# Kernel tuning notes

Hardware: AMD Instinct MI355X
Metric: run time of the kernel (lower is better)

Reference implementation:

```python
import jax, jax.numpy as jnp
import numpy as np
from functools import partial

B, N, T = 4, 10000, 128
E = 160000
H, C = 4, 64            # heads, out_channels per head
GAT_DIM = H * C         # 256
NEG_SLOPE = 0.2


def conv1d(x, w, b):
    # x: (M, Cin, L), w: (Cout, Cin, K), 'same' padding (pad=1 for k=3)
    y = jax.lax.conv_general_dilated(x, w, window_strides=(1,), padding=[(1, 1)],
                                     dimension_numbers=('NCH', 'OIH', 'NCH'))
    return y + b[None, :, None]


def maxpool2(x):
    # kernel=2, stride=2 over last axis
    return jax.lax.reduce_window(x, -jnp.inf, jax.lax.max,
                                 (1, 1, 2), (1, 1, 2), 'VALID')


def gat_layer_single(x, src, dst, W, att_s, att_d, bias):
    # x: (N, Fin); PyG GATConv with concat=True, self-loops already appended to src/dst
    n = x.shape[0]
    xl = (x @ W).reshape(n, H, C)                       # (N, H, C)
    a_s = jnp.sum(xl * att_s[None], axis=-1)            # (N, H)
    a_d = jnp.sum(xl * att_d[None], axis=-1)            # (N, H)
    e = jax.nn.leaky_relu(a_s[src] + a_d[dst], NEG_SLOPE)  # (E', H)
    emax = jax.ops.segment_max(e, dst, num_segments=n)     # (N, H)
    ex = jnp.exp(e - emax[dst])
    denom = jax.ops.segment_sum(ex, dst, num_segments=n)   # (N, H)
    alpha = ex / (denom[dst] + 1e-16)                       # (E', H)
    msg = xl[src] * alpha[..., None]                        # (E', H, C)
    out = jax.ops.segment_sum(msg, dst, num_segments=n)     # (N, H, C)
    return out.reshape(n, H * C) + bias


def setup_inputs() -> dict:
    key = jax.random.key(0)
    ks = jax.random.split(key, 24)
    rn = lambda k, sh, fan: jax.random.normal(k, sh, jnp.float32) / np.sqrt(fan)
    inp = {
        'x': jax.random.normal(ks[0], (B, N, T), jnp.float32),
        'edge_index': jax.random.randint(ks[1], (2, E), 0, N, jnp.int64),
        # temporal conv
        'cw1': rn(ks[2], (32, 1, 3), 3), 'cb1': jnp.zeros((32,), jnp.float32),
        'cw2': rn(ks[3], (64, 32, 3), 96), 'cb2': jnp.zeros((64,), jnp.float32),
        # GAT layer 0 (in=64)
        'W0': rn(ks[4], (64, GAT_DIM), 64), 'as0': rn(ks[5], (H, C), C), 'ad0': rn(ks[6], (H, C), C),
        'b0': jnp.zeros((GAT_DIM,), jnp.float32),
        # GAT layer 1 (in=256)
        'W1': rn(ks[7], (GAT_DIM, GAT_DIM), GAT_DIM), 'as1': rn(ks[8], (H, C), C), 'ad1': rn(ks[9], (H, C), C),
        'b1': jnp.zeros((GAT_DIM,), jnp.float32),
        # classification head 256->128->2
        'Wc1': rn(ks[10], (GAT_DIM, 128), GAT_DIM), 'bc1': jnp.zeros((128,), jnp.float32),
        'Wc2': rn(ks[11], (128, 2), 128), 'bc2': jnp.zeros((2,), jnp.float32),
        # attribution head 256->64->1
        'Wa1': rn(ks[12], (GAT_DIM, 64), GAT_DIM), 'ba1': jnp.zeros((64,), jnp.float32),
        'Wa2': rn(ks[13], (64, 1), 64), 'ba2': jnp.zeros((1,), jnp.float32),
    }
    return inp


def reference(x, edge_index, cw1, cb1, cw2, cb2, W0, as0, ad0, b0, W1, as1, ad1, b1,
              Wc1, bc1, Wc2, bc2, Wa1, ba1, Wa2, ba2):
    b, n, t = x.shape
    # ---- temporal conv over all B*N node signals ----
    xf = x.reshape(b * n, 1, t)
    h = jax.nn.relu(conv1d(xf, cw1, cb1))            # (BN, 32, T)
    h = maxpool2(h)                                  # (BN, 32, T//2)
    h = jax.nn.relu(conv1d(h, cw2, cb2))             # (BN, 64, T//2)
    feat = jnp.mean(h, axis=-1).reshape(b, n, 64)    # adaptive_avg_pool1d(1)
    # ---- GAT stack (self-loops appended, PyG default) ----
    src0, dst0 = edge_index[0], edge_index[1]
    loops = jnp.arange(n, dtype=src0.dtype)
    src = jnp.concatenate([src0, loops])
    dst = jnp.concatenate([dst0, loops])
    gat0 = jax.vmap(partial(gat_layer_single, src=src, dst=dst, W=W0, att_s=as0, att_d=ad0, bias=b0))
    gat1 = jax.vmap(partial(gat_layer_single, src=src, dst=dst, W=W1, att_s=as1, att_d=ad1, bias=b1))
    g = jax.nn.relu(gat0(feat))                      # (B, N, 256); dropout = identity (eval)
    g = jax.nn.relu(gat1(g))                         # (B, N, 256)
    # ---- heads ----
    pooled = jnp.mean(g, axis=1)                     # (B, 256)
    logits = jax.nn.relu(pooled @ Wc1 + bc1) @ Wc2 + bc2          # (B, 2)
    attr = jax.nn.sigmoid(jax.nn.relu(g @ Wa1 + ba1) @ Wa2 + ba2)  # (B, N, 1)
    return logits, attr[..., 0]
```

## Files before the change

kernel.cpp:

```cpp
#include <hip/hip_runtime.h>
#include <hip/hip_bf16.h>
#include <math.h>

typedef __hip_bfloat16 bf16;
typedef unsigned short u16;
typedef unsigned int u32;
typedef __attribute__((ext_vector_type(8))) short short8;
typedef __attribute__((ext_vector_type(4))) float f32x4;
typedef __attribute__((ext_vector_type(2))) float f32x2;

#define BATCH 4
#define NNODE 10000
#define TLEN 128
#define NEDGE 160000
#define GDIM 256
#define NHEAD 4

#define S_CW1 0
#define S_CB1 96
#define S_CB2 128
#define S_AS0 192
#define S_AD0 448
#define S_B0  704
#define S_AS1 960
#define S_AD1 1216
#define S_B1  1472
#define S_BC1 1728
#define S_WC2 1856
#define S_BC2 2112
#define S_BA1 2114
#define S_WA2 2178
#define S_BA2 2242
#define S_TOTAL 2243

__device__ __forceinline__ float prelu(float v) { return 0.5f * (v + fabsf(v)); }
__device__ __forceinline__ u16 f2b(float f) {
    union { float f; u32 u; } v; v.f = f;
    u32 r = v.u + 0x7FFF + ((v.u >> 16) & 1);
    return (u16)(r >> 16);
}
__device__ __forceinline__ float u2f(u16 u) {
    union { u32 u; float f; } v; v.u = ((u32)u) << 16;
    return v.f;
}
__device__ __forceinline__ float ldw(const void* p, int off, bool isbf) {
    return isbf ? u2f(((const u16*)p)[off]) : ((const float*)p)[off];
}

__device__ __forceinline__ bool probe_x_bf16(const void* xsrc) {
    int lane = threadIdx.x & 63;
    u16 h = ((const u16*)xsrc)[2 * lane];
    int e = (h >> 7) & 0xFF;
    unsigned long long m = __ballot(e >= 117 && e <= 130);
    return __popcll(m) >= 32;
}
__device__ __forceinline__ bool probe_ei64(const int* ei) {
    int lane = threadIdx.x & 63;
    int v = ei[2 * lane + 1];
    unsigned long long m = __ballot(v == 0);
    return __popcll(m) >= 56;
}

struct WPtrs { const void* p[20]; };

#define PRE_TBLK 665
__global__ __launch_bounds__(256) void k_pre(WPtrs wp, const void* __restrict__ xsrc,
        const int* __restrict__ ei, float* __restrict__ wbuf,
        u16* __restrict__ cw2r, u16* __restrict__ W0t, u16* __restrict__ W1t,
        u16* __restrict__ Wa1t, int* __restrict__ counts) {
    bool isbf = probe_x_bf16(xsrc);
    int b = blockIdx.x;
    if (b >= PRE_TBLK) {
        const int C2[16] = {0,96,128,192,448,704,960,1216,1472,1728,1856,2112,
                            2114,2178,2242,2243};
        const int SRC[15] = {0,1,3,5,6,7,9,10,11,13,14,15,17,18,19};
        int i = (b - PRE_TBLK) * 256 + threadIdx.x;
        if (i >= S_TOTAL) return;
        int j = 14;
        for (int t = 0; t < 15; ++t) { if (i < C2[t + 1]) { j = t; break; } }
        wbuf[i] = ldw(wp.p[SRC[j]], i - C2[j], isbf);
        return;
    }
    int i = b * 256 + threadIdx.x;
    if (i < 6144) {
        int c2 = i / 96, k = i - c2 * 96, s = k >> 5, ci = k & 31;
        cw2r[i] = f2b(ldw(wp.p[2], c2 * 96 + ci * 3 + s, isbf));
    }
    if (i < 16384) {
        int k = i >> 8, c = i & 255;
        W0t[c * 64 + k] = f2b(ldw(wp.p[4], k * 256 + c, isbf));
        int ka = i >> 6, ca = i & 63;
        Wa1t[ca * 256 + ka] = f2b(ldw(wp.p[16], ka * 64 + ca, isbf));
    }
    if (i < 65536) {
        int k = i >> 8, c = i & 255;
        W1t[c * 256 + k] = f2b(ldw(wp.p[8], k * 256 + c, isbf));
    }
    if (i < NEDGE + NNODE) {
        bool ei64 = probe_ei64(ei);
        int dst;
        if (i < NEDGE) dst = ei64 ? ei[2 * (NEDGE + i)] : ei[NEDGE + i];
        else dst = i - NEDGE;
        if (dst >= 0 && dst < NNODE) atomicAdd(&counts[dst], 1);
    }
}

__global__ __launch_bounds__(256) void k_scan1(const int* __restrict__ counts,
        int* __restrict__ cur, int* __restrict__ bsum) {
    __shared__ int buf[256];
    int tid = threadIdx.x;
    int i = blockIdx.x * 256 + tid;
    int v = (i < NNODE) ? counts[i] : 0;
    buf[tid] = v;
    __syncthreads();
    for (int off = 1; off < 256; off <<= 1) {
        int t = (tid >= off) ? buf[tid - off] : 0;
        __syncthreads();
        buf[tid] += t;
        __syncthreads();
    }
    if (i < NNODE) cur[i] = buf[tid];
    if (tid == 255) bsum[blockIdx.x] = buf[255];
}
__global__ __launch_bounds__(256) void k_scan3(const int* __restrict__ counts,
        int* __restrict__ cur, const int* __restrict__ bsum, int* __restrict__ row_ptr) {
    __shared__ int pre_s;
    int tid = threadIdx.x;
    if (tid == 0) {
        int s = 0;
        for (int j = 0; j < blockIdx.x; ++j) s += bsum[j];
        pre_s = s;
    }
    __syncthreads();
    int i = blockIdx.x * 256 + tid;
    if (i >= NNODE) return;
    int incl = cur[i] + pre_s;
    row_ptr[i + 1] = incl;
    cur[i] = incl - counts[i];
    if (i == 0) row_ptr[0] = 0;
}

#define HSTR 40
#define WSTR 96
#define FILL_BLK 665
__global__ __launch_bounds__(256) void k_conv(const void* __restrict__ xsrc,
        const float* __restrict__ wbuf, const u16* __restrict__ cw2r,
        u16* __restrict__ featb, const int* __restrict__ ei,
        int* __restrict__ cur, int* __restrict__ col_src) {
    __shared__ __align__(16) float xs[4][132];
    __shared__ float w1s[96], b1s[32], b2s[64];
    __shared__ __align__(16) u16 w2s[64 * WSTR];
    __shared__ __align__(16) u16 hs[66 * HSTR];
    __shared__ float red2[4][64];

    bool isbf = probe_x_bf16(xsrc);
    int tid = threadIdx.x;
    int wave = tid >> 6, lane = tid & 63;
    int node0 = blockIdx.x * 4;

    {
        int j = tid >> 6, p = (tid & 63) * 2;
        if (isbf) {
            u32 w = ((const u32*)xsrc)[(size_t)node0 * 64 + tid];
            xs[j][1 + p] = u2f((u16)(w & 0xFFFF));
            xs[j][2 + p] = u2f((u16)(w >> 16));
        } else {
            float2 w = ((const float2*)xsrc)[(size_t)node0 * 64 + tid];
            xs[j][1 + p] = w.x;
            xs[j][2 + p] = w.y;
        }
    }
    if (tid < 8) xs[tid >> 1][(tid & 1) ? 129 : 0] = 0.f;
    if (tid < 96) w1s[tid] = wbuf[S_CW1 + tid];
    if (tid < 32) b1s[tid] = wbuf[S_CB1 + tid];
    if (tid < 64) b2s[tid] = wbuf[S_CB2 + tid];
    for (int i = tid; i < 768; i += 256)
        ((short8*)w2s)[i] = ((const short8*)cw2r)[i];
    if (tid < 32) hs[tid] = 0;
    else if (tid < 64) hs[65 * HSTR + (tid - 32)] = 0;
    __syncthreads();

    int d = tid & 15, uu = tid >> 4;
    float wa0 = w1s[6 * d + 0], wa1 = w1s[6 * d + 1], wa2 = w1s[6 * d + 2];
    float wb0 = w1s[6 * d + 3], wb1 = w1s[6 * d + 4], wb2 = w1s[6 * d + 5];
    float ba = b1s[2 * d], bb = b1s[2 * d + 1];
    int m = lane & 15, q = lane >> 4;
    int trow = wave * 16 + m;

    for (int j = 0; j < 4; ++j) {
        const float* xr = &xs[j][0];
        #pragma unroll
        for (int it = 0; it < 4; ++it) {
            int u = uu + 16 * it;
            int t0 = 2 * u;
            float x0 = xr[t0], x1 = xr[t0 + 1], x2 = xr[t0 + 2], x3 = xr[t0 + 3];
            f32x2 A = {x0, x1}, Bv = {x1, x2}, Cv = {x2, x3};
            f32x2 va = {ba, ba}; va += wa0 * A; va += wa1 * Bv; va += wa2 * Cv;
            f32x2 vb = {bb, bb}; vb += wb0 * A; vb += wb1 * Bv; vb += wb2 * Cv;
            float ha = fmaxf(fmaxf(va.x, va.y), 0.f);
            float hb = fmaxf(fmaxf(vb.x, vb.y), 0.f);
            __hip_bfloat162 hp2 = __float22bfloat162_rn(make_float2(ha, hb));
            u32 pack; __builtin_memcpy(&pack, &hp2, 4);
            *(u32*)&hs[(u + 1) * HSTR + 2 * d] = pack;
        }
        __syncthreads();

        short8 afr[3];
        #pragma unroll
        for (int s = 0; s < 3; ++s)
            afr[s] = *(const short8*)&hs[(trow + s) * HSTR + q * 8];
        float psum[4];
        #pragma unroll
        for (int nt = 0; nt < 4; ++nt) {
            int n = nt * 16 + m;
            f32x4 acc = {0.f, 0.f, 0.f, 0.f};
            #pragma unroll
            for (int s = 0; s < 3; ++s) {
                short8 bfr = *(const short8*)&w2s[n * WSTR + s * 32 + q * 8];
                acc = __builtin_amdgcn_mfma_f32_16x16x32_bf16(afr[s], bfr, acc, 0, 0, 0);
            }
            float b2v = b2s[n];
            float scl = prelu(acc[0] + b2v) + prelu(acc[1] + b2v)
                      + prelu(acc[2] + b2v) + prelu(acc[3] + b2v);
            scl += __shfl_xor(scl, 16, 64);
            scl += __shfl_xor(scl, 32, 64);
            psum[nt] = scl;
        }
        if (lane < 16) {
            #pragma unroll
            for (int nt = 0; nt < 4; ++nt)
                red2[wave][nt * 16 + lane] = psum[nt];
        }
        __syncthreads();
        if (tid < 64) {
            float tot = (red2[0][tid] + red2[1][tid] + red2[2][tid] + red2[3][tid]) * (1.f / 64.f);
            int node = node0 + j;
            int bb2 = node / NNODE, nn = node - bb2 * NNODE;
            featb[((size_t)nn * 4 + bb2) * 64 + tid] = f2b(tot);
        }
    }

    if (blockIdx.x < FILL_BLK) {
        bool ei64 = probe_ei64(ei);
        int e = blockIdx.x * 256 + tid;
        if (e < NEDGE + NNODE) {
            int src, dst;
            if (e < NEDGE) {
                if (ei64) { src = ei[2 * e]; dst = ei[2 * (NEDGE + e)]; }
                else      { src = ei[e];     dst = ei[NEDGE + e]; }
            } else {
                src = dst = e - NEDGE;
            }
            if (dst >= 0 && dst < NNODE) {
                int pos = atomicAdd(&cur[dst], 1);
                if (pos >= 0 && pos < NEDGE + NNODE) col_src[pos] = src;
            }
        }
    }
}

template<int K>
__global__ __launch_bounds__(256) void k_gemm(const u16* __restrict__ A,
        const u16* __restrict__ Wt, const float* __restrict__ att_s_w,
        const float* __restrict__ att_d_w, u16* __restrict__ outb,
        float* __restrict__ a_s, float* __restrict__ a_d) {
    int wave = threadIdx.x >> 6, lane = threadIdx.x & 63;
    int row0 = (blockIdx.x * 4 + wave) * 16;
    int m = lane & 15, q = lane >> 4;
    f32x4 acc[16];
    #pragma unroll
    for (int nt = 0; nt < 16; ++nt) acc[nt] = {0.f, 0.f, 0.f, 0.f};
    for (int kc = 0; kc < K; kc += 32) {
        short8 a = *(const short8*)&A[(size_t)(row0 + m) * K + kc + q * 8];
        #pragma unroll
        for (int nt = 0; nt < 16; ++nt) {
            short8 b = *(const short8*)&Wt[(size_t)(nt * 16 + m) * K + kc + q * 8];
            acc[nt] = __builtin_amdgcn_mfma_f32_16x16x32_bf16(a, b, acc[nt], 0, 0, 0);
        }
    }
    #pragma unroll
    for (int nt = 0; nt < 16; ++nt) {
        #pragma unroll
        for (int r = 0; r < 4; ++r)
            outb[(size_t)(row0 + q * 4 + r) * 256 + nt * 16 + m] = f2b(acc[nt][r]);
    }
    float sh_s[4][4] = {{0}}, sh_d[4][4] = {{0}};
    #pragma unroll
    for (int nt = 0; nt < 16; ++nt) {
        int h = nt >> 2;
        int cc = (nt & 3) * 16 + m;
        float asw = att_s_w[h * 64 + cc];
        float adw = att_d_w[h * 64 + cc];
        #pragma unroll
        for (int r = 0; r < 4; ++r) {
            sh_s[h][r] += acc[nt][r] * asw;
            sh_d[h][r] += acc[nt][r] * adw;
        }
    }
    #pragma unroll
    for (int off = 1; off < 16; off <<= 1) {
        #pragma unroll
        for (int h = 0; h < 4; ++h)
            #pragma unroll
            for (int r = 0; r < 4; ++r) {
                sh_s[h][r] += __shfl_xor(sh_s[h][r], off, 64);
                sh_d[h][r] += __shfl_xor(sh_d[h][r], off, 64);
            }
    }
    if (m == 0) {
        #pragma unroll
        for (int r = 0; r < 4; ++r) {
            int row = row0 + q * 4 + r;
            float4 vs = {sh_s[0][r], sh_s[1][r], sh_s[2][r], sh_s[3][r]};
            float4 vd = {sh_d[0][r], sh_d[1][r], sh_d[2][r], sh_d[3][r]};
            *(float4*)&a_s[(size_t)row * 4] = vs;
            *(float4*)&a_d[(size_t)row * 4] = vd;
        }
    }
}

__global__ __launch_bounds__(256) void k_agg(const u16* __restrict__ xlb,
        const float* __restrict__ a_s, const float* __restrict__ a_d,
        const int* __restrict__ row_ptr, const int* __restrict__ col_src,
        const float* __restrict__ bias, u16* __restrict__ gb_out) {
    int wave = threadIdx.x >> 6, lane = threadIdx.x & 63;
    int dst = blockIdx.x * 2 + (wave >> 1);
    int bp = (wave & 1) * 2;
    int beg = row_ptr[dst], end = row_ptr[dst + 1];

    int c = lane & 7, g = lane >> 3;
    int bc = bp + (c >> 2), hc = c & 3;
    float adv1 = a_d[(size_t)dst * 16 + bc * 4 + hc];
    float mloc = -INFINITY;
    for (int i = beg + g; i < end; i += 8) {
        int src = min(max(col_src[i], 0), NNODE - 1);
        float e = a_s[(size_t)src * 16 + bc * 4 + hc] + adv1;
        e = (e >= 0.f) ? e : 0.2f * e;
        mloc = fmaxf(mloc, e);
    }
    mloc = fmaxf(mloc, __shfl_xor(mloc, 8, 64));
    mloc = fmaxf(mloc, __shfl_xor(mloc, 16, 64));
    mloc = fmaxf(mloc, __shfl_xor(mloc, 32, 64));

    int bl = lane >> 5;
    int s = lane & 31;
    int h = s >> 3;
    int b = bp + bl;
    float mv = __shfl(mloc, bl * 4 + h, 64);

    float advh = a_d[(size_t)dst * 16 + b * 4 + h];
    float acc[8];
    #pragma unroll
    for (int k = 0; k < 8; ++k) acc[k] = 0.f;
    float l = 0.f;

    int asoff = b * 4 + h;
    int i = beg;
    for (; i + 4 <= end; i += 4) {
        int s0 = min(max(col_src[i], 0), NNODE - 1);
        int s1 = min(max(col_src[i + 1], 0), NNODE - 1);
        int s2 = min(max(col_src[i + 2], 0), NNODE - 1);
        int s3 = min(max(col_src[i + 3], 0), NNODE - 1);
        float a0 = a_s[(size_t)s0 * 16 + asoff];
        float a1 = a_s[(size_t)s1 * 16 + asoff];
        float a2 = a_s[(size_t)s2 * 16 + asoff];
        float a3 = a_s[(size_t)s3 * 16 + asoff];
        short8 x0 = *(const short8*)&xlb[((size_t)s0 * 4 + b) * 256 + s * 8];
        short8 x1 = *(const short8*)&xlb[((size_t)s1 * 4 + b) * 256 + s * 8];
        short8 x2 = *(const short8*)&xlb[((size_t)s2 * 4 + b) * 256 + s * 8];
        short8 x3 = *(const short8*)&xlb[((size_t)s3 * 4 + b) * 256 + s * 8];
        float e0 = a0 + advh; e0 = (e0 >= 0.f) ? e0 : 0.2f * e0;
        float p0 = __expf(e0 - mv); l += p0;
        #pragma unroll
        for (int k = 0; k < 8; ++k) acc[k] += p0 * u2f((u16)x0[k]);
        float e1 = a1 + advh; e1 = (e1 >= 0.f) ? e1 : 0.2f * e1;
        float p1 = __expf(e1 - mv); l += p1;
        #pragma unroll
        for (int k = 0; k < 8; ++k) acc[k] += p1 * u2f((u16)x1[k]);
        float e2 = a2 + advh; e2 = (e2 >= 0.f) ? e2 : 0.2f * e2;
        float p2 = __expf(e2 - mv); l += p2;
        #pragma unroll
        for (int k = 0; k < 8; ++k) acc[k] += p2 * u2f((u16)x2[k]);
        float e3 = a3 + advh; e3 = (e3 >= 0.f) ? e3 : 0.2f * e3;
        float p3 = __expf(e3 - mv); l += p3;
        #pragma unroll
        for (int k = 0; k < 8; ++k) acc[k] += p3 * u2f((u16)x3[k]);
    }
    for (; i < end; ++i) {
        int s0 = min(max(col_src[i], 0), NNODE - 1);
        float a0 = a_s[(size_t)s0 * 16 + asoff];
        short8 x0 = *(const short8*)&xlb[((size_t)s0 * 4 + b) * 256 + s * 8];
        float e0 = a0 + advh; e0 = (e0 >= 0.f) ? e0 : 0.2f * e0;
        float p0 = __expf(e0 - mv); l += p0;
        #pragma unroll
        for (int k = 0; k < 8; ++k) acc[k] += p0 * u2f((u16)x0[k]);
    }
    float rl = 1.f / (l + 1e-16f);
    short8 o;
    #pragma unroll
    for (int k = 0; k < 8; ++k)
        o[k] = (short)f2b(prelu(acc[k] * rl + bias[s * 8 + k]));
    *(short8*)&gb_out[((size_t)dst * 4 + b) * 256 + s * 8] = o;
}

__global__ __launch_bounds__(256) void k_attrpool(const u16* __restrict__ gb,
        const u16* __restrict__ Wa1t, const float* __restrict__ wbuf,
        float* __restrict__ out, float* __restrict__ pooled) {
    if (blockIdx.x >= 625) {
        int pb = blockIdx.x - 625;
        int b = pb >> 6;
        int chunk = pb & 63;
        int cch = threadIdx.x;
        int n0 = chunk * 157;
        int n1 = min(NNODE, n0 + 157);
        float acc = 0.f;
        int n = n0;
        for (; n + 4 <= n1; n += 4) {
            float v0 = u2f(gb[((size_t)n * 4 + b) * 256 + cch]);
            float v1 = u2f(gb[((size_t)(n + 1) * 4 + b) * 256 + cch]);
            float v2 = u2f(gb[((size_t)(n + 2) * 4 + b) * 256 + cch]);
            float v3 = u2f(gb[((size_t)(n + 3) * 4 + b) * 256 + cch]);
            acc += v0; acc += v1; acc += v2; acc += v3;
        }
        for (; n < n1; ++n)
            acc += u2f(gb[((size_t)n * 4 + b) * 256 + cch]);
        atomicAdd(&pooled[b * 256 + cch], acc);
        return;
    }
    int wave = threadIdx.x >> 6, lane = threadIdx.x & 63;
    int row0 = (blockIdx.x * 4 + wave) * 16;
    int m = lane & 15, q = lane >> 4;
    f32x4 acc[4];
    #pragma unroll
    for (int nt = 0; nt < 4; ++nt) acc[nt] = {0.f, 0.f, 0.f, 0.f};
    for (int kc = 0; kc < 256; kc += 32) {
        short8 a = *(const short8*)&gb[(size_t)(row0 + m) * 256 + kc + q * 8];
        #pragma unroll
        for (int nt = 0; nt < 4; ++nt) {
            short8 b = *(const short8*)&Wa1t[(size_t)(nt * 16 + m) * 256 + kc + q * 8];
            acc[nt] = __builtin_amdgcn_mfma_f32_16x16x32_bf16(a, b, acc[nt], 0, 0, 0);
        }
    }
    float part[4] = {0, 0, 0, 0};
    #pragma unroll
    for (int nt = 0; nt < 4; ++nt) {
        int col = nt * 16 + m;
        float ba1v = wbuf[S_BA1 + col];
        float wa2v = wbuf[S_WA2 + col];
        #pragma unroll
        for (int r = 0; r < 4; ++r)
            part[r] += prelu(acc[nt][r] + ba1v) * wa2v;
    }
    #pragma unroll
    for (int off = 1; off < 16; off <<= 1) {
        #pragma unroll
        for (int r = 0; r < 4; ++r)
            part[r] += __shfl_xor(part[r], off, 64);
    }
    if (m == 0) {
        float ba2v = wbuf[S_BA2];
        #pragma unroll
        for (int r = 0; r < 4; ++r) {
            int row = row0 + q * 4 + r;
            int n = row >> 2, b = row & 3;
            float v = part[r] + ba2v;
            out[8 + b * NNODE + n] = 1.f / (1.f + __expf(-v));
        }
    }
}

__global__ __launch_bounds__(128) void k_logits(const float* __restrict__ pooled,
        const float* __restrict__ wbuf, const void* __restrict__ Wc1p,
        float* __restrict__ out,
        const u16* __restrict__ featb, const u16* __restrict__ gb,
        const int* __restrict__ row_ptr, const int* __restrict__ ei,
        const void* __restrict__ xsrc, int hostbad) {
    int tid = threadIdx.x;
    bool isbf = probe_x_bf16(xsrc);
    if (blockIdx.x == 4) {
        __shared__ float red[128];
        bool ei64 = probe_ei64(ei);
        float mx[2] = {0.f, 0.f};
        const u16* bufs[2] = {featb, gb};
        for (int qq = 0; qq < 2; ++qq) {
            const u16* p = bufs[qq];
            float m = 0.f;
            for (int i = tid; i < 2048; i += 128) {
                float v = u2f(p[i]);
                if (v != v) m = 1e30f;
                m = fmaxf(m, fabsf(v));
            }
            red[tid] = m;
            __syncthreads();
            for (int s2 = 64; s2 > 0; s2 >>= 1) {
                if (tid < s2) red[tid] = fmaxf(red[tid], red[tid + s2]);
                __syncthreads();
            }
            mx[qq] = red[0];
            __syncthreads();
        }
        if (tid == 0) {
            int fb = (mx[0] > 1e8f || mx[0] < 1e-6f) ? 1 : 0;
            int gbad = (mx[1] > 1e8f || mx[1] < 1e-6f) ? 1 : 0;
            int cb = (row_ptr[NNODE] != NEDGE + NNODE) ? 1 : 0;
            int code = 100 * fb + 400 * gbad + 800 * cb + 6400 * hostbad;
            if (code) {
                code += 1600 * (isbf ? 0 : 1);
                code += 3200 * (ei64 ? 1 : 0);
                for (int j = 0; j < 8; ++j) out[j] = (float)code;
            }
        }
        return;
    }
    __shared__ float pm[256];
    __shared__ float red4[4];
    int b = blockIdx.x;
    pm[tid] = pooled[b * 256 + tid] * (1.f / NNODE);
    pm[tid + 128] = pooled[b * 256 + tid + 128] * (1.f / NNODE);
    __syncthreads();
    float acc = wbuf[S_BC1 + tid];
    if (isbf) {
        const u16* w = (const u16*)Wc1p;
        #pragma unroll 4
        for (int k = 0; k < 256; ++k)
            acc += pm[k] * u2f(w[k * 128 + tid]);
    } else {
        const float* w = (const float*)Wc1p;
        #pragma unroll 4
        for (int k = 0; k < 256; ++k)
            acc += pm[k] * w[k * 128 + tid];
    }
    float hv = prelu(acc);
    float p0 = hv * wbuf[S_WC2 + tid * 2];
    float p1 = hv * wbuf[S_WC2 + tid * 2 + 1];
    #pragma unroll
    for (int off = 32; off > 0; off >>= 1) {
        p0 += __shfl_xor(p0, off, 64);
        p1 += __shfl_xor(p1, off, 64);
    }
    int wv = tid >> 6, lane = tid & 63;
    if (lane == 0) { red4[wv * 2] = p0; red4[wv * 2 + 1] = p1; }
    __syncthreads();
    if (tid < 2)
        out[b * 2 + tid] = red4[tid] + red4[2 + tid] + wbuf[S_BC2 + tid];
}

extern "C" void kernel_launch(void* const* d_in, const int* in_sizes, int n_in,
                              void* d_out, int out_size, void* d_ws, size_t ws_size,
                              hipStream_t stream) {
    const void* x  = d_in[0];
    const int*  ei = (const int*)d_in[1];
    float* out = (float*)d_out;

    WPtrs wp;
    for (int j = 0; j < 20; ++j) wp.p[j] = d_in[j + 2];

    char* ws = (char*)d_ws;
    size_t off = 0;
    auto alloc = [&](size_t bytes) -> void* {
        void* p = ws + off;
        off += (bytes + 255) & ~(size_t)255;
        return p;
    };
    float* wbuf    = (float*)alloc((size_t)S_TOTAL * 4);
    u16*   featb   = (u16*)  alloc((size_t)BATCH * NNODE * 64 * 2);
    u16*   xlb     = (u16*)  alloc((size_t)BATCH * NNODE * 256 * 2);
    u16*   gb      = (u16*)  alloc((size_t)BATCH * NNODE * 256 * 2);
    float* a_s     = (float*)alloc((size_t)BATCH * NNODE * 4 * 4);
    float* a_d     = (float*)alloc((size_t)BATCH * NNODE * 4 * 4);
    u16*   cw2r    = (u16*)alloc(6144 * 2);
    u16*   W0t     = (u16*)alloc(16384 * 2);
    u16*   W1t     = (u16*)alloc(65536 * 2);
    u16*   Wa1t    = (u16*)alloc(16384 * 2);
    int*   counts  = (int*)alloc(NNODE * 4);
    float* pooled  = (float*)alloc(BATCH * 256 * 4);
    int*   row_ptr = (int*)alloc((NNODE + 1) * 4);
    int*   cur     = (int*)alloc(NNODE * 4);
    int*   col_src = (int*)alloc((NEDGE + NNODE) * 4);
    int*   bsum    = (int*)alloc(64 * 4);
    (void)ws_size; (void)out_size;

    int hostbad = (n_in != 22 || in_sizes[0] != BATCH * NNODE * TLEN ||
                   in_sizes[1] != 2 * NEDGE) ? 1 : 0;

    hipMemsetAsync(counts, 0, 40192 + 4096, stream);

    k_pre<<<PRE_TBLK + 9, 256, 0, stream>>>(wp, x, ei, wbuf, cw2r, W0t, W1t, Wa1t, counts);
    k_scan1<<<40, 256, 0, stream>>>(counts, cur, bsum);
    k_scan3<<<40, 256, 0, stream>>>(counts, cur, bsum, row_ptr);

    k_conv<<<BATCH * NNODE / 4, 256, 0, stream>>>(x, wbuf, cw2r, featb, ei, cur, col_src);

    k_gemm<64><<<BATCH * NNODE / 64, 256, 0, stream>>>(featb, W0t,
            wbuf + S_AS0, wbuf + S_AD0, xlb, a_s, a_d);
    k_agg<<<NNODE / 2, 256, 0, stream>>>(xlb, a_s, a_d, row_ptr, col_src, wbuf + S_B0, gb);

    k_gemm<256><<<BATCH * NNODE / 64, 256, 0, stream>>>(gb, W1t,
            wbuf + S_AS1, wbuf + S_AD1, xlb, a_s, a_d);
    k_agg<<<NNODE / 2, 256, 0, stream>>>(xlb, a_s, a_d, row_ptr, col_src, wbuf + S_B1, gb);

    k_attrpool<<<625 + 256, 256, 0, stream>>>(gb, Wa1t, wbuf, out, pooled);
    k_logits<<<5, 128, 0, stream>>>(pooled, wbuf, wp.p[12], out, featb, gb, row_ptr, ei, x, hostbad);
}
```

Baseline: 418.3 us.

## Split conv2 work by output channel per wave and double-buffer the hidden tile

Each wave now computes 16 output channels across all 64 time rows, instead of 16 time rows across all 64 channels. The per-channel mean can then be reduced inside the wave with no shared-memory reduction buffer. The hidden activation buffer is double-buffered, which removes the second __syncthreads per node iteration. This cuts barriers and LDS traffic in the conv kernel, at the cost of more LDS A-fragment loads per wave and more accumulator registers.

```diff
diff --git a/kernel.cpp b/kernel.cpp
--- a/kernel.cpp
+++ b/kernel.cpp
@@ -150,8 +150,7 @@
     __shared__ __align__(16) float xs[4][132];
     __shared__ float w1s[96], b1s[32], b2s[64];
     __shared__ __align__(16) u16 w2s[64 * WSTR];
-    __shared__ __align__(16) u16 hs[66 * HSTR];
-    __shared__ float red2[4][64];
+    __shared__ __align__(16) u16 hs[2][66 * HSTR];
 
     bool isbf = probe_x_bf16(xsrc);
     int tid = threadIdx.x;
@@ -176,8 +175,10 @@
     if (tid < 64) b2s[tid] = wbuf[S_CB2 + tid];
     for (int i = tid; i < 768; i += 256)
         ((short8*)w2s)[i] = ((const short8*)cw2r)[i];
-    if (tid < 32) hs[tid] = 0;
-    else if (tid < 64) hs[65 * HSTR + (tid - 32)] = 0;
+    if (tid < 128) {
+        int bf = tid >> 6, seg = (tid >> 5) & 1, ch = tid & 31;
+        hs[bf][seg ? (65 * HSTR + ch) : ch] = 0;
+    }
     __syncthreads();
 
     int d = tid & 15, uu = tid >> 4;
@@ -185,9 +186,11 @@
     float wb0 = w1s[6 * d + 3], wb1 = w1s[6 * d + 4], wb2 = w1s[6 * d + 5];
     float ba = b1s[2 * d], bb = b1s[2 * d + 1];
     int m = lane & 15, q = lane >> 4;
-    int trow = wave * 16 + m;
+    int n = wave * 16 + m;
+    float b2v = b2s[n];
 
     for (int j = 0; j < 4; ++j) {
+        u16* hw = &hs[j & 1][0];
         const float* xr = &xs[j][0];
         #pragma unroll
         for (int it = 0; it < 4; ++it) {
@@ -201,42 +204,38 @@
             float hb = fmaxf(fmaxf(vb.x, vb.y), 0.f);
             __hip_bfloat162 hp2 = __float22bfloat162_rn(make_float2(ha, hb));
             u32 pack; __builtin_memcpy(&pack, &hp2, 4);
-            *(u32*)&hs[(u + 1) * HSTR + 2 * d] = pack;
+            *(u32*)&hw[(u + 1) * HSTR + 2 * d] = pack;
         }
         __syncthreads();
 
-        short8 afr[3];
-        #pragma unroll
-        for (int s = 0; s < 3; ++s)
-            afr[s] = *(const short8*)&hs[(trow + s) * HSTR + q * 8];
-        float psum[4];
-        #pragma unroll
-        for (int nt = 0; nt < 4; ++nt) {
-            int n = nt * 16 + m;
-            f32x4 acc = {0.f, 0.f, 0.f, 0.f};
-            #pragma unroll
-            for (int s = 0; s < 3; ++s) {
-                short8 bfr = *(const short8*)&w2s[n * WSTR + s * 32 + q * 8];
-                acc = __builtin_amdgcn_mfma_f32_16x16x32_bf16(afr[s], bfr, acc, 0, 0, 0);
-            }
-            float b2v = b2s[n];
-            float scl = prelu(acc[0] + b2v) + prelu(acc[1] + b2v)
-                      + prelu(acc[2] + b2v) + prelu(acc[3] + b2v);
-            scl += __shfl_xor(scl, 16, 64);
-            scl += __shfl_xor(scl, 32, 64);
-            psum[nt] = scl;
-        }
+        f32x4 accm0 = {0.f,0.f,0.f,0.f}, accm1 = {0.f,0.f,0.f,0.f};
+        f32x4 accm2 = {0.f,0.f,0.f,0.f}, accm3 = {0.f,0.f,0.f,0.f};
+        #pragma unroll
+        for (int s = 0; s < 3; ++s) {
+            short8 bfr = *(const short8*)&w2s[n * WSTR + s * 32 + q * 8];
+            short8 a0 = *(const short8*)&hw[(0 * 16 + m + s) * HSTR + q * 8];
+            short8 a1 = *(const short8*)&hw[(1 * 16 + m + s) * HSTR + q * 8];
+            short8 a2 = *(const short8*)&hw[(2 * 16 + m + s) * HSTR + q * 8];
+            short8 a3 = *(const short8*)&hw[(3 * 16 + m + s) * HSTR + q * 8];
+            accm0 = __builtin_amdgcn_mfma_f32_16x16x32_bf16(a0, bfr, accm0, 0, 0, 0);
+            accm1 = __builtin_amdgcn_mfma_f32_16x16x32_bf16(a1, bfr, accm1, 0, 0, 0);
+            accm2 = __builtin_amdgcn_mfma_f32_16x16x32_bf16(a2, bfr, accm2, 0, 0, 0);
+            accm3 = __builtin_amdgcn_mfma_f32_16x16x32_bf16(a3, bfr, accm3, 0, 0, 0);
+        }
+        float scl = prelu(accm0[0] + b2v) + prelu(accm0[1] + b2v)
+                  + prelu(accm0[2] + b2v) + prelu(accm0[3] + b2v);
+        scl += prelu(accm1[0] + b2v) + prelu(accm1[1] + b2v)
+             + prelu(accm1[2] + b2v) + prelu(accm1[3] + b2v);
+        scl += prelu(accm2[0] + b2v) + prelu(accm2[1] + b2v)
+             + prelu(accm2[2] + b2v) + prelu(accm2[3] + b2v);
+        scl += prelu(accm3[0] + b2v) + prelu(accm3[1] + b2v)
+             + prelu(accm3[2] + b2v) + prelu(accm3[3] + b2v);
+        scl += __shfl_xor(scl, 16, 64);
+        scl += __shfl_xor(scl, 32, 64);
         if (lane < 16) {
-            #pragma unroll
-            for (int nt = 0; nt < 4; ++nt)
-                red2[wave][nt * 16 + lane] = psum[nt];
-        }
-        __syncthreads();
-        if (tid < 64) {
-            float tot = (red2[0][tid] + red2[1][tid] + red2[2][tid] + red2[3][tid]) * (1.f / 64.f);
             int node = node0 + j;
             int bb2 = node / NNODE, nn = node - bb2 * NNODE;
-            featb[((size_t)nn * 4 + bb2) * 64 + tid] = f2b(tot);
+            featb[((size_t)nn * 4 + bb2) * 64 + wave * 16 + lane] = f2b(scl * (1.f / 64.f));
         }
     }
 
```

Result: no change. 414.4 us (-0.9%).
